# Kernel optimization log

Hardware: AMD Instinct MI355X
Metric: run time of the kernel (lower is better)

The kernel has to match this reference:

```python
import jax, jax.numpy as jnp
import numpy as np

S = 2048          # sequence length (single prefill sequence)
HID = 4096        # hidden_size
NH, NKV, HD = 32, 8, 128   # q heads, kv heads, head_dim
THETA = 10000.0
SCALE = HD ** -0.5


def setup_inputs() -> dict:
    key = jax.random.key(0)
    k1, k2, k3 = jax.random.split(key, 3)
    hidden_states = jax.random.normal(k1, (S, HID), jnp.float32)
    positions = jnp.arange(S, dtype=jnp.int32)
    W_qkv = jax.random.normal(k2, (HID, (NH + 2 * NKV) * HD), jnp.float32) * 0.02
    W_o = jax.random.normal(k3, (NH * HD, HID), jnp.float32) * 0.02
    return {"hidden_states": hidden_states, "positions": positions,
            "W_qkv": W_qkv, "W_o": W_o}


def _rope(x, positions):
    # x: [T, H, HD]; neox-style RoPE (rotate halves, is_neox_style=True)
    half = HD // 2
    inv_freq = 1.0 / (THETA ** (jnp.arange(half, dtype=jnp.float32) / half))
    freqs = positions.astype(jnp.float32)[:, None] * inv_freq[None, :]  # [T, half]
    cos = jnp.cos(freqs)[:, None, :]
    sin = jnp.sin(freqs)[:, None, :]
    x1, x2 = x[..., :half], x[..., half:]
    return jnp.concatenate([x1 * cos - x2 * sin, x2 * cos + x1 * sin], axis=-1)


def reference(hidden_states, positions, W_qkv, W_o):
    # fused QKV projection then split (q_size = NH*HD, kv_size = NKV*HD)
    qkv = hidden_states @ W_qkv                      # [S, (NH+2*NKV)*HD]
    q, k, v = jnp.split(qkv, [NH * HD, NH * HD + NKV * HD], axis=1)
    q = _rope(q.reshape(S, NH, HD), positions)       # [S, NH, HD]
    k = _rope(k.reshape(S, NKV, HD), positions)      # [S, NKV, HD]
    v = v.reshape(S, NKV, HD)
    # GQA: broadcast kv heads to query heads
    rep = NH // NKV
    k = jnp.repeat(k, rep, axis=1)                   # [S, NH, HD]
    v = jnp.repeat(v, rep, axis=1)
    scores = jnp.einsum('qhd,khd->hqk', q, k) * SCALE  # [NH, S, S]
    causal = jnp.tril(jnp.ones((S, S), dtype=bool))
    scores = jnp.where(causal[None], scores, jnp.finfo(scores.dtype).min)
    attn = jax.nn.softmax(scores, axis=-1)
    out = jnp.einsum('hqk,khd->qhd', attn, v).reshape(S, NH * HD)
    return out @ W_o                                 # [S, HID]
```

## Files before the change

### kernel.cpp

```cpp
#include <hip/hip_runtime.h>
#include <math.h>
#include <stdint.h>

#define S_LEN 2048
#define HID 4096
#define NH 32
#define NKV 8
#define HD 128
#define QKV_N ((NH + 2*NKV) * HD)
#define NQK (NH + NKV)
static __device__ __constant__ const float SCALE_F = 0.08838834764831845f;

typedef __bf16 bf16x8 __attribute__((ext_vector_type(8)));
typedef __bf16 bf16x4 __attribute__((ext_vector_type(4)));
typedef float  f32x4  __attribute__((ext_vector_type(4)));
typedef uint32_t u32x4 __attribute__((ext_vector_type(4)));

#define GLD_LDS(gptr, lptr) \
  __builtin_amdgcn_global_load_lds( \
      (const __attribute__((address_space(1))) uint32_t*)(gptr), \
      (__attribute__((address_space(3))) uint32_t*)(lptr), 16, 0, 0)

__global__ void cast_bf16_kernel(const float4* __restrict__ in, __bf16* __restrict__ out, int n4) {
  int i = blockIdx.x * blockDim.x + threadIdx.x;
  if (i >= n4) return;
  float4 v = in[i];
  bf16x4 o = { (__bf16)v.x, (__bf16)v.y, (__bf16)v.z, (__bf16)v.w };
  *(bf16x4*)(out + (size_t)i * 4) = o;
}

__global__ void add_f32_kernel(const float4* __restrict__ a, const float4* __restrict__ b,
                               float4* __restrict__ o, int n4) {
  int i = blockIdx.x * blockDim.x + threadIdx.x;
  int stride = gridDim.x * blockDim.x;
  for (; i < n4; i += stride) {
    float4 x = a[i], y = b[i];
    float4 r; r.x = x.x + y.x; r.y = x.y + y.y; r.z = x.z + y.z; r.w = x.w + y.w;
    o[i] = r;
  }
}

__global__ void transpose_cast_kernel(const float* __restrict__ in, __bf16* __restrict__ out,
                                      int R, int C) {
  __shared__ float tile[32][33];
  int bx = blockIdx.x * 32;
  int by = blockIdx.y * 32;
  int tx = threadIdx.x, ty = threadIdx.y;
  for (int i = 0; i < 32; i += 8)
    tile[ty + i][tx] = in[(size_t)(by + ty + i) * C + bx + tx];
  __syncthreads();
  for (int i = 0; i < 32; i += 8)
    out[(size_t)(bx + ty + i) * R + by + tx] = (__bf16)tile[tx][ty + i];
}

__global__ void transpose_v_kernel(const __bf16* __restrict__ qkv, __bf16* __restrict__ Vt) {
  __shared__ __bf16 tile[32][33];
  int kvh = blockIdx.z;
  int sb = blockIdx.x * 32;
  int db = blockIdx.y * 32;
  int tx = threadIdx.x, ty = threadIdx.y;
  const __bf16* src = qkv + (size_t)(NH + NKV) * HD + (size_t)kvh * HD;
  for (int i = 0; i < 32; i += 8)
    tile[ty + i][tx] = src[(size_t)(sb + ty + i) * QKV_N + db + tx];
  __syncthreads();
  for (int i = 0; i < 32; i += 8)
    Vt[((size_t)kvh * HD + db + ty + i) * S_LEN + sb + tx] = tile[tx][ty + i];
}

__global__ void rope_kernel(const __bf16* __restrict__ qkv, const int* __restrict__ pos,
                            __bf16* __restrict__ Qr, __bf16* __restrict__ Kr) {
  int idx = blockIdx.x * blockDim.x + threadIdx.x;
  int half = idx & 63;
  int t = idx >> 6;
  int hh = t % NQK;
  int s = t / NQK;
  if (s >= S_LEN) return;
  float p = (float)pos[s];
  float inv_freq = exp2f((float)half * -0.2076205059304601f);
  float ang = p * inv_freq;
  float cs = cosf(ang), sn = sinf(ang);
  const __bf16* src; __bf16* dst;
  if (hh < NH) {
    src = qkv + (size_t)s * QKV_N + (size_t)hh * HD;
    dst = Qr + ((size_t)s * NH + hh) * HD;
  } else {
    int kh = hh - NH;
    src = qkv + (size_t)s * QKV_N + (size_t)NH * HD + (size_t)kh * HD;
    dst = Kr + ((size_t)s * NKV + kh) * HD;
  }
  float x1 = (float)src[half], x2 = (float)src[half + 64];
  dst[half]      = (__bf16)(x1 * cs - x2 * sn);
  dst[half + 64] = (__bf16)(x2 * cs + x1 * sn);
}

template <typename OutT>
__global__ __launch_bounds__(512, 2) void gemm8p_kernel(const __bf16* __restrict__ A,
                                                        const __bf16* __restrict__ Bt,
                                                        OutT* __restrict__ C0,
                                                        OutT* __restrict__ C1,
                                                        int M, int N, int Kext, int ld) {
  __shared__ __align__(16) __bf16 sA[2][2][256 * 32];
  __shared__ __align__(16) __bf16 sB[2][2][256 * 32];
  const int tid = threadIdx.x;
  const int lane = tid & 63;
  const int wave = tid >> 6;
  const int quad = lane >> 4;
  const int l16 = lane & 15;
  const int wm = (wave >> 2) * 128;
  const int wn = (wave & 3) * 64;

  const int z = blockIdx.z;
  A += (size_t)z * Kext;
  Bt += (size_t)z * Kext;
  OutT* __restrict__ C = z ? C1 : C0;

  const int nx = gridDim.x;
  size_t bm, bn;
  if (gridDim.y == 8 && (nx & 7) == 0) {
    int lin = blockIdx.y * nx + blockIdx.x;
    int j = lin >> 3, xcd = lin & 7;
    bm = (size_t)(j & 7) * 256;
    bn = (size_t)(xcd * (nx >> 3) + (j >> 3)) * 256;
  } else {
    bm = (size_t)blockIdx.y * 256;
    bn = (size_t)blockIdx.x * 256;
  }

  const int NT = Kext >> 6;
  const int rsw = (l16 >> 1) & 3;

  f32x4 acc[8][4] = {};
  bf16x8 aR[2][4], bR[2][4];

  const int row0 = tid >> 2;
  const int chL = (tid & 3) ^ ((tid >> 3) & 3);
  const uint64_t off128 = (uint64_t)128 * ld * 2;
  uint64_t aGA = (uint64_t)(uintptr_t)A + ((bm + row0) * (size_t)ld) * 2 + (size_t)chL * 16;
  uint64_t bGA = (uint64_t)(uintptr_t)Bt + ((bn + row0) * (size_t)ld) * 2 + (size_t)chL * 16;

  typedef __attribute__((address_space(3))) __bf16 lds_bf16;
  const uint32_t sAb = (uint32_t)(uintptr_t)(lds_bf16*)&sA[0][0][0];
  const uint32_t sBb = (uint32_t)(uintptr_t)(lds_bf16*)&sB[0][0][0];
  const uint32_t wlds = (uint32_t)__builtin_amdgcn_readfirstlane(wave * 1024);
  const uint32_t aBase = sAb + (uint32_t)(((wm + l16) * 32 + (quad ^ rsw) * 8) * 2);
  const uint32_t bBase = sBb + (uint32_t)(((wn + l16) * 32 + (quad ^ rsw) * 8) * 2);

#define LDSA(bf, kk) (sAb + (bf) * 32768u + (kk) * 16384u)
#define LDSB(bf, kk) (sBb + (bf) * 32768u + (kk) * 16384u)

#define STAGE_ASM(ga, ldsbase) \
  asm volatile("s_mov_b32 m0, %0\n\t" \
               "global_load_lds_dwordx4 %2, off\n\t" \
               "s_mov_b32 m0, %1\n\t" \
               "global_load_lds_dwordx4 %3, off" \
               :: "s"((ldsbase) + wlds), "s"((ldsbase) + wlds + 8192u), \
                  "v"(ga), "v"((ga) + off128) : "memory")

#define DSRD4(dst, baseaddr) do {                                                 \
    u32x4 t0_, t1_, t2_, t3_;                                                     \
    asm volatile("ds_read_b128 %0, %4\n\t"                                        \
                 "ds_read_b128 %1, %4 offset:1024\n\t"                            \
                 "ds_read_b128 %2, %4 offset:2048\n\t"                            \
                 "ds_read_b128 %3, %4 offset:3072"                                \
                 : "=&v"(t0_), "=&v"(t1_), "=&v"(t2_), "=&v"(t3_)                 \
                 : "v"(baseaddr));                                                \
    dst[0] = __builtin_bit_cast(bf16x8, t0_);                                     \
    dst[1] = __builtin_bit_cast(bf16x8, t1_);                                     \
    dst[2] = __builtin_bit_cast(bf16x8, t2_);                                     \
    dst[3] = __builtin_bit_cast(bf16x8, t3_);                                     \
  } while (0)

#define ISSUE_A(set, bf, kk, ih) DSRD4(aR[set], aBase + (bf) * 32768u + (kk) * 16384u + (ih) * 4096u)
#define ISSUE_B(set, bf, kk)     DSRD4(bR[set], bBase + (bf) * 32768u + (kk) * 16384u)

#define MFMA16(as, bs, ih) do {                                                   \
    __builtin_amdgcn_s_setprio(1);                                                \
    _Pragma("unroll")                                                             \
    for (int i_ = 0; i_ < 4; ++i_)                                                \
      _Pragma("unroll")                                                           \
      for (int j_ = 0; j_ < 4; ++j_)                                              \
        acc[(ih) * 4 + i_][j_] = __builtin_amdgcn_mfma_f32_16x16x32_bf16(         \
            aR[as][i_], bR[bs][j_], acc[(ih) * 4 + i_][j_], 0, 0, 0);             \
    __builtin_amdgcn_s_setprio(0);                                                \
    __builtin_amdgcn_sched_barrier(0);                                            \
  } while (0)

#define BAR() __builtin_amdgcn_s_barrier()
#define LGKM4() do { asm volatile("s_waitcnt lgkmcnt(4)");                        \
                     __builtin_amdgcn_sched_barrier(0); } while (0)
#define LGKM8() do { asm volatile("s_waitcnt lgkmcnt(8)");                        \
                     __builtin_amdgcn_sched_barrier(0); } while (0)
#define VMCNT4() do { asm volatile("s_waitcnt vmcnt(4)");                         \
                      __builtin_amdgcn_sched_barrier(0); } while (0)

  STAGE_ASM(aGA,        LDSA(0, 0));
  STAGE_ASM(bGA,        LDSB(0, 0));
  STAGE_ASM(aGA + 64,   LDSA(0, 1));
  STAGE_ASM(bGA + 64,   LDSB(0, 1));
  STAGE_ASM(aGA + 128,  LDSA(1, 0));
  STAGE_ASM(bGA + 128,  LDSB(1, 0));
  aGA += 192; bGA += 192;
  asm volatile("s_waitcnt vmcnt(8)");
  __builtin_amdgcn_sched_barrier(0);
  BAR();
  ISSUE_A(0, 0, 0, 0); ISSUE_B(0, 0, 0);

  for (int u = 0; u < (NT >> 1); ++u) {
    VMCNT4();
    ISSUE_A(1, 0, 0, 1);
    BAR();
    LGKM4();
    MFMA16(0, 0, 0);
    STAGE_ASM(aGA, LDSA(1, 1)); aGA += 64;
    ISSUE_A(0, 0, 1, 0); ISSUE_B(1, 0, 1);
    BAR();
    LGKM8();
    MFMA16(1, 0, 1);
    STAGE_ASM(bGA, LDSB(1, 1)); bGA += 64;
    VMCNT4();
    ISSUE_A(1, 0, 1, 1);
    BAR();
    LGKM4();
    MFMA16(0, 1, 0);
    STAGE_ASM(aGA, LDSA(0, 0)); aGA += 64;
    ISSUE_A(0, 1, 0, 0); ISSUE_B(0, 1, 0);
    BAR();
    LGKM8();
    MFMA16(1, 1, 1);
    STAGE_ASM(bGA, LDSB(0, 0)); bGA += 64;
    VMCNT4();
    ISSUE_A(1, 1, 0, 1);
    BAR();
    LGKM4();
    MFMA16(0, 0, 0);
    STAGE_ASM(aGA, LDSA(0, 1)); aGA += 64;
    ISSUE_A(0, 1, 1, 0); ISSUE_B(1, 1, 1);
    BAR();
    LGKM8();
    MFMA16(1, 0, 1);
    STAGE_ASM(bGA, LDSB(0, 1)); bGA += 64;
    VMCNT4();
    ISSUE_A(1, 1, 1, 1);
    BAR();
    LGKM4();
    MFMA16(0, 1, 0);
    STAGE_ASM(aGA, LDSA(1, 0)); aGA += 64;
    ISSUE_A(0, 0, 0, 0); ISSUE_B(0, 0, 0);
    BAR();
    LGKM8();
    MFMA16(1, 1, 1);
    STAGE_ASM(bGA, LDSB(1, 0)); bGA += 64;
  }

  asm volatile("s_waitcnt vmcnt(0) lgkmcnt(0)");
  __builtin_amdgcn_sched_barrier(0);

  #pragma unroll
  for (int i = 0; i < 8; ++i)
    #pragma unroll
    for (int j = 0; j < 4; ++j)
      #pragma unroll
      for (int r = 0; r < 4; ++r) {
        size_t row = bm + wm + i * 16 + quad * 4 + r;
        size_t col = bn + wn + j * 16 + l16;
        C[row * (size_t)N + col] = (OutT)acc[i][j][r];
      }

#undef LDSA
#undef LDSB
#undef STAGE_ASM
#undef DSRD4
#undef ISSUE_A
#undef ISSUE_B
#undef MFMA16
#undef BAR
#undef LGKM4
#undef LGKM8
#undef VMCNT4
}

__global__ __launch_bounds__(256, 2) void attn_kernel(const __bf16* __restrict__ Qr,
                                                      const __bf16* __restrict__ Kr,
                                                      const __bf16* __restrict__ Vt,
                                                      __bf16* __restrict__ O) {
  __shared__ __align__(16) char smem[73728];
  __bf16* Ps = (__bf16*)(smem + 65536);

  const int bid = blockIdx.x;
  const int h = bid & (NH - 1);
  const int qb = (S_LEN / 64 - 1) - (bid >> 5);
  const int kvh = h >> 2;
  const int tid = threadIdx.x;
  const int lane = tid & 63, wave = tid >> 6;
  const int quad = lane >> 4, l16 = lane & 15;
  const int sw = l16 & 7;
  const int q0 = qb * 64;

#define STAGE_KV(kbase, bufv) do {                                                 \
    char* kd_ = smem + (bufv) * 16384;                                             \
    char* vd_ = smem + 32768 + (bufv) * 16384;                                     \
    _Pragma("unroll")                                                              \
    for (int pass_ = 0; pass_ < 4; ++pass_) {                                      \
      int c_ = pass_ * 256 + tid;                                                  \
      int row_ = c_ >> 4, ch_ = c_ & 15;                                           \
      int chs_ = ch_ ^ (row_ & 7);                                                 \
      GLD_LDS(&Kr[(size_t)((kbase) + row_) * (NKV * HD) + (size_t)kvh * HD + chs_ * 8], \
              kd_ + c_ * 16);                                                      \
    }                                                                              \
    _Pragma("unroll")                                                              \
    for (int pass_ = 0; pass_ < 4; ++pass_) {                                      \
      int c_ = pass_ * 256 + tid;                                                  \
      int d_ = c_ >> 3, ch_ = c_ & 7;                                              \
      int chs_ = ch_ ^ (d_ & 7);                                                   \
      GLD_LDS(&Vt[((size_t)kvh * HD + d_) * S_LEN + (kbase) + chs_ * 8],           \
              vd_ + c_ * 16);                                                      \
    }                                                                              \
  } while (0)

  bf16x8 qf[4];
  {
    const __bf16* qp = Qr + (size_t)(q0 + wave * 16 + l16) * (NH * HD) + (size_t)h * HD + quad * 8;
    for (int kk = 0; kk < 4; ++kk) qf[kk] = *(const bf16x8*)(qp + kk * 32);
  }
  f32x4 oacc[8] = {};
  float m2 = -INFINITY, l_i = 0.0f;
  const float C2 = SCALE_F * 1.4426950408889634f;

  int buf = 0;
  STAGE_KV(0, 0);
  for (int kb = 0; kb <= q0; kb += 64) {
    __syncthreads();
    if (kb + 64 <= q0) STAGE_KV(kb + 64, buf ^ 1);

    const __bf16* Ks = (const __bf16*)(smem + buf * 16384);
    const __bf16* Vs = (const __bf16*)(smem + 32768 + buf * 16384);

    f32x4 sc[4] = {};
    __builtin_amdgcn_s_setprio(1);
    for (int jt = 0; jt < 4; ++jt)
      for (int kk = 0; kk < 4; ++kk) {
        bf16x8 kf = *(const bf16x8*)&Ks[(jt * 16 + l16) * 128 + ((kk * 4 + quad) ^ sw) * 8];
        sc[jt] = __builtin_amdgcn_mfma_f32_16x16x32_bf16(kf, qf[kk], sc[jt], 0, 0, 0);
      }
    __builtin_amdgcn_s_setprio(0);

    float s[16];
    for (int jt = 0; jt < 4; ++jt)
      for (int r = 0; r < 4; ++r) s[jt * 4 + r] = sc[jt][r];
    if (kb == q0) {
      int qloc = wave * 16 + l16;
      for (int jt = 0; jt < 4; ++jt)
        for (int r = 0; r < 4; ++r)
          if (jt * 16 + quad * 4 + r > qloc) s[jt * 4 + r] = -INFINITY;
    }
    float mx = s[0];
    for (int i = 1; i < 16; ++i) mx = fmaxf(mx, s[i]);
    mx = fmaxf(mx, __shfl_xor(mx, 16, 64));
    mx = fmaxf(mx, __shfl_xor(mx, 32, 64));
    float m2new = fmaxf(m2, mx * C2);
    float alpha = exp2f(m2 - m2new);
    float pv[16], sum = 0.0f;
    for (int i = 0; i < 16; ++i) { pv[i] = exp2f(fmaf(s[i], C2, -m2new)); sum += pv[i]; }
    sum += __shfl_xor(sum, 16, 64);
    sum += __shfl_xor(sum, 32, 64);
    l_i = l_i * alpha + sum;
    m2 = m2new;
    for (int dt = 0; dt < 8; ++dt) oacc[dt] *= alpha;

    __bf16* pw = Ps + wave * 1024 + l16 * 64;
    for (int jt = 0; jt < 4; ++jt) {
      bf16x4 pk = { (__bf16)pv[jt*4+0], (__bf16)pv[jt*4+1], (__bf16)pv[jt*4+2], (__bf16)pv[jt*4+3] };
      int chunk = jt * 2 + (quad >> 1);
      *(bf16x4*)&pw[((chunk ^ sw) * 8) + (quad & 1) * 4] = pk;
    }
    __builtin_amdgcn_s_setprio(1);
    for (int half = 0; half < 2; ++half) {
      bf16x8 pf = *(const bf16x8*)&pw[((half * 4 + quad) ^ sw) * 8];
      for (int dt = 0; dt < 8; ++dt) {
        bf16x8 vf = *(const bf16x8*)&Vs[(dt * 16 + l16) * 64 + ((half * 4 + quad) ^ sw) * 8];
        oacc[dt] = __builtin_amdgcn_mfma_f32_16x16x32_bf16(vf, pf, oacc[dt], 0, 0, 0);
      }
    }
    __builtin_amdgcn_s_setprio(0);
    buf ^= 1;
  }
  __syncthreads();

#undef STAGE_KV

  float* scr = (float*)smem + wave * 2112;
  float inv = 1.0f / l_i;
  for (int dt = 0; dt < 8; ++dt) {
    f32x4 v = oacc[dt] * inv;
    *(f32x4*)&scr[l16 * 132 + dt * 16 + quad * 4] = v;
  }
  for (int it = 0; it < 4; ++it) {
    int c = it * 64 + lane;
    int row = c >> 4, ch = c & 15;
    const float* sp = &scr[row * 132 + ch * 8];
    f32x4 a = *(const f32x4*)sp;
    f32x4 b = *(const f32x4*)(sp + 4);
    bf16x8 o = { (__bf16)a[0], (__bf16)a[1], (__bf16)a[2], (__bf16)a[3],
                 (__bf16)b[0], (__bf16)b[1], (__bf16)b[2], (__bf16)b[3] };
    *(bf16x8*)&O[(size_t)(q0 + wave * 16 + row) * (NH * HD) + (size_t)h * HD + ch * 8] = o;
  }
}

extern "C" void kernel_launch(void* const* d_in, const int* in_sizes, int n_in,
                              void* d_out, int out_size, void* d_ws, size_t ws_size,
                              hipStream_t stream) {
  const float* hidden    = (const float*)d_in[0];
  const int*   positions = (const int*)d_in[1];
  const float* Wqkv      = (const float*)d_in[2];
  const float* Wo        = (const float*)d_in[3];
  float* out = (float*)d_out;

  char* p = (char*)d_ws;
  auto alloc = [&](size_t bytes) { char* r = p; p += (bytes + 255) & ~(size_t)255; return r; };
  __bf16* hid_bf = (__bf16*)alloc((size_t)S_LEN * HID * 2);
  __bf16* wqkvT  = (__bf16*)alloc((size_t)QKV_N * HID * 2);
  __bf16* woT    = (__bf16*)alloc((size_t)HID * HID * 2);
  __bf16* qkv    = (__bf16*)alloc((size_t)S_LEN * QKV_N * 2);
  __bf16* Qr     = (__bf16*)alloc((size_t)S_LEN * NH * HD * 2);
  __bf16* Kr     = (__bf16*)alloc((size_t)S_LEN * NKV * HD * 2);
  __bf16* Vt     = (__bf16*)alloc((size_t)S_LEN * NKV * HD * 2);
  __bf16* attn   = hid_bf;

  float* Cp0 = (float*)wqkvT;
  float* Cp1 = (float*)qkv;

  {
    int n4 = S_LEN * HID / 4;
    cast_bf16_kernel<<<(n4 + 255) / 256, 256, 0, stream>>>((const float4*)hidden, hid_bf, n4);
  }
  transpose_cast_kernel<<<dim3(QKV_N / 32, HID / 32), dim3(32, 8), 0, stream>>>(Wqkv, wqkvT, HID, QKV_N);
  transpose_cast_kernel<<<dim3(HID / 32, HID / 32), dim3(32, 8), 0, stream>>>(Wo, woT, HID, HID);
  gemm8p_kernel<__bf16><<<dim3(QKV_N / 256, S_LEN / 256, 1), 512, 0, stream>>>(
      hid_bf, wqkvT, qkv, qkv, S_LEN, QKV_N, HID, HID);
  {
    int total = S_LEN * NQK * 64;
    rope_kernel<<<total / 256, 256, 0, stream>>>(qkv, positions, Qr, Kr);
  }
  transpose_v_kernel<<<dim3(S_LEN / 32, HD / 32, NKV), dim3(32, 8), 0, stream>>>(qkv, Vt);
  attn_kernel<<<NH * (S_LEN / 64), 256, 0, stream>>>(Qr, Kr, Vt, attn);
  gemm8p_kernel<float><<<dim3(HID / 256, S_LEN / 256, 2), 512, 0, stream>>>(
      attn, woT, Cp0, Cp1, S_LEN, HID, HID / 2, HID);
  {
    int n4 = S_LEN * HID / 4;
    add_f32_kernel<<<2048, 256, 0, stream>>>((const float4*)Cp0, (const float4*)Cp1,
                                             (float4*)out, n4);
  }
}
```

Baseline: 505.0 us.

## Fuse prep and rope/V-transpose kernels, drop split-K, add lazy softmax rescale

Merges the hidden cast and both weight transposes into one launch, with a wider 64x64 float4 transpose tile. Also merges RoPE with the V transpose, and removes the split-K output GEMM and its add kernel by writing the output GEMM straight to the result. In attention, the running max and accumulator rescale are updated only when a wave's new max exceeds the old one by a threshold. This cuts launches and the partial-buffer traffic but lowers output-GEMM parallelism to 128 blocks, and lazy rescaling risks overflow only past the threshold.

```diff
diff --git a/kernel.cpp b/kernel.cpp
--- a/kernel.cpp
+++ b/kernel.cpp
@@ -21,76 +21,103 @@
       (const __attribute__((address_space(1))) uint32_t*)(gptr), \
       (__attribute__((address_space(3))) uint32_t*)(lptr), 16, 0, 0)
 
-__global__ void cast_bf16_kernel(const float4* __restrict__ in, __bf16* __restrict__ out, int n4) {
-  int i = blockIdx.x * blockDim.x + threadIdx.x;
-  if (i >= n4) return;
-  float4 v = in[i];
-  bf16x4 o = { (__bf16)v.x, (__bf16)v.y, (__bf16)v.z, (__bf16)v.w };
-  *(bf16x4*)(out + (size_t)i * 4) = o;
-}
-
-__global__ void add_f32_kernel(const float4* __restrict__ a, const float4* __restrict__ b,
-                               float4* __restrict__ o, int n4) {
-  int i = blockIdx.x * blockDim.x + threadIdx.x;
-  int stride = gridDim.x * blockDim.x;
-  for (; i < n4; i += stride) {
-    float4 x = a[i], y = b[i];
-    float4 r; r.x = x.x + y.x; r.y = x.y + y.y; r.z = x.z + y.z; r.w = x.w + y.w;
-    o[i] = r;
-  }
-}
-
-__global__ void transpose_cast_kernel(const float* __restrict__ in, __bf16* __restrict__ out,
-                                      int R, int C) {
-  __shared__ float tile[32][33];
-  int bx = blockIdx.x * 32;
-  int by = blockIdx.y * 32;
-  int tx = threadIdx.x, ty = threadIdx.y;
-  for (int i = 0; i < 32; i += 8)
-    tile[ty + i][tx] = in[(size_t)(by + ty + i) * C + bx + tx];
+__device__ __forceinline__ void tp64(const float* __restrict__ in, __bf16* __restrict__ out,
+                                     int R, int C, int bx, int by, int tid, float* tile) {
+  int lr = tid >> 4;
+  int lc = (tid & 15) * 4;
+  #pragma unroll
+  for (int p = 0; p < 4; ++p) {
+    int r = p * 16 + lr;
+    const float4 v = *(const float4*)&in[(size_t)(by + r) * C + bx + lc];
+    float* t = &tile[r * 65 + lc];
+    t[0] = v.x; t[1] = v.y; t[2] = v.z; t[3] = v.w;
+  }
   __syncthreads();
-  for (int i = 0; i < 32; i += 8)
-    out[(size_t)(bx + ty + i) * R + by + tx] = (__bf16)tile[tx][ty + i];
-}
-
-__global__ void transpose_v_kernel(const __bf16* __restrict__ qkv, __bf16* __restrict__ Vt) {
+  int oc = tid >> 5;
+  int orr = (tid & 31) * 2;
+  #pragma unroll
+  for (int p = 0; p < 8; ++p) {
+    int c = p * 8 + oc;
+    float v0 = tile[orr * 65 + c];
+    float v1 = tile[(orr + 1) * 65 + c];
+    __bf16 b2[2] = { (__bf16)v0, (__bf16)v1 };
+    *(uint32_t*)&out[(size_t)(bx + c) * R + by + orr] = *(uint32_t*)b2;
+  }
+}
+
+__global__ __launch_bounds__(256) void fused_prep_kernel(const float* __restrict__ hidden,
+                                                         __bf16* __restrict__ hid_bf,
+                                                         const float* __restrict__ Wqkv,
+                                                         __bf16* __restrict__ wqkvT,
+                                                         const float* __restrict__ Wo,
+                                                         __bf16* __restrict__ woT) {
+  __shared__ float tile[64 * 65];
+  const int b = blockIdx.x;
+  const int tid = threadIdx.x;
+  if (b < 2048) {
+    const float4* in4 = (const float4*)hidden;
+    int i = b * 256 + tid;
+    #pragma unroll
+    for (int k = 0; k < 4; ++k) {
+      float4 v = in4[i + k * 524288];
+      bf16x4 o = { (__bf16)v.x, (__bf16)v.y, (__bf16)v.z, (__bf16)v.w };
+      *(bf16x4*)(hid_bf + (size_t)(i + k * 524288) * 4) = o;
+    }
+  } else if (b < 8192) {
+    int id = b - 2048;
+    int bx = (id % 96) * 64, by = (id / 96) * 64;
+    tp64(Wqkv, wqkvT, HID, QKV_N, bx, by, tid, tile);
+  } else {
+    int id = b - 8192;
+    int bx = (id & 63) * 64, by = (id >> 6) * 64;
+    tp64(Wo, woT, HID, HID, bx, by, tid, tile);
+  }
+}
+
+__global__ __launch_bounds__(256) void fused_rope_tpv_kernel(const __bf16* __restrict__ qkv,
+                                                             const int* __restrict__ pos,
+                                                             __bf16* __restrict__ Qr,
+                                                             __bf16* __restrict__ Kr,
+                                                             __bf16* __restrict__ Vt) {
   __shared__ __bf16 tile[32][33];
-  int kvh = blockIdx.z;
-  int sb = blockIdx.x * 32;
-  int db = blockIdx.y * 32;
-  int tx = threadIdx.x, ty = threadIdx.y;
-  const __bf16* src = qkv + (size_t)(NH + NKV) * HD + (size_t)kvh * HD;
-  for (int i = 0; i < 32; i += 8)
-    tile[ty + i][tx] = src[(size_t)(sb + ty + i) * QKV_N + db + tx];
-  __syncthreads();
-  for (int i = 0; i < 32; i += 8)
-    Vt[((size_t)kvh * HD + db + ty + i) * S_LEN + sb + tx] = tile[tx][ty + i];
-}
-
-__global__ void rope_kernel(const __bf16* __restrict__ qkv, const int* __restrict__ pos,
-                            __bf16* __restrict__ Qr, __bf16* __restrict__ Kr) {
-  int idx = blockIdx.x * blockDim.x + threadIdx.x;
-  int half = idx & 63;
-  int t = idx >> 6;
-  int hh = t % NQK;
-  int s = t / NQK;
-  if (s >= S_LEN) return;
-  float p = (float)pos[s];
-  float inv_freq = exp2f((float)half * -0.2076205059304601f);
-  float ang = p * inv_freq;
-  float cs = cosf(ang), sn = sinf(ang);
-  const __bf16* src; __bf16* dst;
-  if (hh < NH) {
-    src = qkv + (size_t)s * QKV_N + (size_t)hh * HD;
-    dst = Qr + ((size_t)s * NH + hh) * HD;
+  const int b = blockIdx.x;
+  const int tid = threadIdx.x;
+  if (b < 20480) {
+    int idx = b * 256 + tid;
+    int half = idx & 63;
+    int t = idx >> 6;
+    int hh = t % NQK;
+    int s = t / NQK;
+    if (s >= S_LEN) return;
+    float p = (float)pos[s];
+    float inv_freq = exp2f((float)half * -0.2076205059304601f);
+    float ang = p * inv_freq;
+    float cs = cosf(ang), sn = sinf(ang);
+    const __bf16* src; __bf16* dst;
+    if (hh < NH) {
+      src = qkv + (size_t)s * QKV_N + (size_t)hh * HD;
+      dst = Qr + ((size_t)s * NH + hh) * HD;
+    } else {
+      int kh = hh - NH;
+      src = qkv + (size_t)s * QKV_N + (size_t)NH * HD + (size_t)kh * HD;
+      dst = Kr + ((size_t)s * NKV + kh) * HD;
+    }
+    float x1 = (float)src[half], x2 = (float)src[half + 64];
+    dst[half]      = (__bf16)(x1 * cs - x2 * sn);
+    dst[half + 64] = (__bf16)(x2 * cs + x1 * sn);
   } else {
-    int kh = hh - NH;
-    src = qkv + (size_t)s * QKV_N + (size_t)NH * HD + (size_t)kh * HD;
-    dst = Kr + ((size_t)s * NKV + kh) * HD;
-  }
-  float x1 = (float)src[half], x2 = (float)src[half + 64];
-  dst[half]      = (__bf16)(x1 * cs - x2 * sn);
-  dst[half + 64] = (__bf16)(x2 * cs + x1 * sn);
+    int id = b - 20480;
+    int sb = (id & 63) * 32;
+    int db = ((id >> 6) & 3) * 32;
+    int kvh = id >> 8;
+    int tx = tid & 31, ty = tid >> 5;
+    const __bf16* src = qkv + (size_t)(NH + NKV) * HD + (size_t)kvh * HD;
+    for (int i = 0; i < 32; i += 8)
+      tile[ty + i][tx] = src[(size_t)(sb + ty + i) * QKV_N + db + tx];
+    __syncthreads();
+    for (int i = 0; i < 32; i += 8)
+      Vt[((size_t)kvh * HD + db + ty + i) * S_LEN + sb + tx] = tile[tx][ty + i];
+  }
 }
 
 template <typename OutT>
@@ -357,15 +384,19 @@
     for (int i = 1; i < 16; ++i) mx = fmaxf(mx, s[i]);
     mx = fmaxf(mx, __shfl_xor(mx, 16, 64));
     mx = fmaxf(mx, __shfl_xor(mx, 32, 64));
-    float m2new = fmaxf(m2, mx * C2);
-    float alpha = exp2f(m2 - m2new);
+    float mxs = mx * C2;
+    if (!__all(mxs <= m2 + 11.54f)) {
+      float m2new = fmaxf(m2, mxs);
+      float alpha = exp2f(m2 - m2new);
+      l_i *= alpha;
+      for (int dt = 0; dt < 8; ++dt) oacc[dt] *= alpha;
+      m2 = m2new;
+    }
     float pv[16], sum = 0.0f;
-    for (int i = 0; i < 16; ++i) { pv[i] = exp2f(fmaf(s[i], C2, -m2new)); sum += pv[i]; }
+    for (int i = 0; i < 16; ++i) { pv[i] = exp2f(fmaf(s[i], C2, -m2)); sum += pv[i]; }
     sum += __shfl_xor(sum, 16, 64);
     sum += __shfl_xor(sum, 32, 64);
-    l_i = l_i * alpha + sum;
-    m2 = m2new;
-    for (int dt = 0; dt < 8; ++dt) oacc[dt] *= alpha;
+    l_i += sum;
 
     __bf16* pw = Ps + wave * 1024 + l16 * 64;
     for (int jt = 0; jt < 4; ++jt) {
@@ -426,28 +457,11 @@
   __bf16* Vt     = (__bf16*)alloc((size_t)S_LEN * NKV * HD * 2);
   __bf16* attn   = hid_bf;
 
-  float* Cp0 = (float*)wqkvT;
-  float* Cp1 = (float*)qkv;
-
-  {
-    int n4 = S_LEN * HID / 4;
-    cast_bf16_kernel<<<(n4 + 255) / 256, 256, 0, stream>>>((const float4*)hidden, hid_bf, n4);
-  }
-  transpose_cast_kernel<<<dim3(QKV_N / 32, HID / 32), dim3(32, 8), 0, stream>>>(Wqkv, wqkvT, HID, QKV_N);
-  transpose_cast_kernel<<<dim3(HID / 32, HID / 32), dim3(32, 8), 0, stream>>>(Wo, woT, HID, HID);
+  fused_prep_kernel<<<12288, 256, 0, stream>>>(hidden, hid_bf, Wqkv, wqkvT, Wo, woT);
   gemm8p_kernel<__bf16><<<dim3(QKV_N / 256, S_LEN / 256, 1), 512, 0, stream>>>(
       hid_bf, wqkvT, qkv, qkv, S_LEN, QKV_N, HID, HID);
-  {
-    int total = S_LEN * NQK * 64;
-    rope_kernel<<<total / 256, 256, 0, stream>>>(qkv, positions, Qr, Kr);
-  }
-  transpose_v_kernel<<<dim3(S_LEN / 32, HD / 32, NKV), dim3(32, 8), 0, stream>>>(qkv, Vt);
+  fused_rope_tpv_kernel<<<22528, 256, 0, stream>>>(qkv, positions, Qr, Kr, Vt);
   attn_kernel<<<NH * (S_LEN / 64), 256, 0, stream>>>(Qr, Kr, Vt, attn);
-  gemm8p_kernel<float><<<dim3(HID / 256, S_LEN / 256, 2), 512, 0, stream>>>(
-      attn, woT, Cp0, Cp1, S_LEN, HID, HID / 2, HID);
-  {
-    int n4 = S_LEN * HID / 4;
-    add_f32_kernel<<<2048, 256, 0, stream>>>((const float4*)Cp0, (const float4*)Cp1,
-                                             (float4*)out, n4);
-  }
-}
+  gemm8p_kernel<float><<<dim3(HID / 256, S_LEN / 256, 1), 512, 0, stream>>>(
+      attn, woT, out, out, S_LEN, HID, HID, HID);
+}
```

Result: faster. 483.9 us (-4.2%).
